# Kernel tuning notes

Measured on AMD Instinct MI355X. Metric: run time of the kernel, lower is better.

Reference implementation:

```python
import jax, jax.numpy as jnp
import numpy as np

NUM_HEADS = 8

def dwconv(x, w, b, pad):
    # depthwise conv: x [B, C, H, W], w [C, 1, k, k], groups=C
    y = jax.lax.conv_general_dilated(
        x, w, window_strides=(1, 1), padding=[(pad, pad), (pad, pad)],
        feature_group_count=x.shape[1], dimension_numbers=('NCHW', 'OIHW', 'NCHW'))
    return y + b[None, :, None, None]


def setup_inputs() -> dict:
    key = jax.random.key(0)
    ks = jax.random.split(key, 12)
    B, H, W = 32, 28, 28
    C = 512
    N = 1 + H * W
    Ch = C // NUM_HEADS  # 64
    s = lambda k, shp, fan: jax.random.normal(k, shp, jnp.float32) * (fan ** -0.5)
    return {
        'x': jax.random.normal(ks[0], (B, N, C), jnp.float32),
        'qkv_w': s(ks[1], (3 * C, C), C),
        'qkv_b': jnp.zeros((3 * C,), jnp.float32),
        'proj_w': s(ks[2], (C, C), C),
        'proj_b': jnp.zeros((C,), jnp.float32),
        'w3': s(ks[3], (2 * Ch, 1, 3, 3), 9),
        'b3': jnp.zeros((2 * Ch,), jnp.float32),
        'w5': s(ks[4], (3 * Ch, 1, 5, 5), 25),
        'b5': jnp.zeros((3 * Ch,), jnp.float32),
        'w7': s(ks[5], (3 * Ch, 1, 7, 7), 49),
        'b7': jnp.zeros((3 * Ch,), jnp.float32),
        'H': H,
        'W': W,
    }


def reference(x, qkv_w, qkv_b, proj_w, proj_b, w3, b3, w5, b5, w7, b7, H, W):
    B, N, C = x.shape
    h = NUM_HEADS
    Ch = C // h
    scale = Ch ** -0.5
    # qkv projection -> q, k, v each [B, h, N, Ch]
    qkv = (x @ qkv_w.T + qkv_b).reshape(B, N, 3, h, Ch).transpose(2, 0, 3, 1, 4)
    q, k, v = qkv[0], qkv[1], qkv[2]
    # factorized attention: softmax over tokens on k, then (k^T v) then q @ ...
    k_sm = jax.nn.softmax(k, axis=2)
    kv = jnp.einsum('bhnc,bhnd->bhcd', k_sm, v)          # [B,h,Ch,Ch]
    factor_att = jnp.einsum('bhnc,bhcd->bhnd', q, kv)    # [B,h,N,Ch]
    # conv relative position encoding (CRPE) on image tokens only
    q_img = q[:, :, 1:, :]                               # [B,h,HW,Ch]
    v_img = v[:, :, 1:, :].transpose(0, 1, 3, 2).reshape(B, h * Ch, H, W)
    splits = np.cumsum([2 * Ch, 3 * Ch, 3 * Ch])[:-1]
    v1, v2, v3 = jnp.split(v_img, splits, axis=1)
    conv_v = jnp.concatenate(
        [dwconv(v1, w3, b3, 1), dwconv(v2, w5, b5, 2), dwconv(v3, w7, b7, 3)], axis=1)
    conv_v = conv_v.reshape(B, h, Ch, H * W).transpose(0, 1, 3, 2)  # [B,h,HW,Ch]
    EV = q_img * conv_v
    crpe = jnp.pad(EV, ((0, 0), (0, 0), (1, 0), (0, 0)))  # zero row for cls token
    out = scale * factor_att + crpe
    out = out.transpose(0, 2, 1, 3).reshape(B, N, C)
    return out @ proj_w.T + proj_b
```

## Files before the change

kernel.cpp:

```cpp
#include <hip/hip_runtime.h>
#include <cstdint>
#include <cstddef>


typedef unsigned short u16;

#define HEADS 8
#define CHD   64
#define CDIM  512
#define NTOK  785
#define BATCH 32
#define MROWS (BATCH * NTOK)
#define MPAD  25344
#define QKVN  1536
#define IMGHW 784
#define KVSPLIT 7

typedef float  f32x4  __attribute__((ext_vector_type(4)));
typedef __bf16 bf16x8 __attribute__((ext_vector_type(8)));

__device__ __forceinline__ u16 f2bf(float f) {
  union { float f; uint32_t u; } x; x.f = f;
  uint32_t r = x.u + 0x7fffu + ((x.u >> 16) & 1u);
  return (u16)(r >> 16);
}
__device__ __forceinline__ float bf2f(u16 u) {
  union { uint32_t u; float f; } x; x.u = ((uint32_t)u) << 16;
  return x.f;
}
__device__ __forceinline__ uint32_t pk2(float a, float b) {
#if __has_builtin(__builtin_amdgcn_cvt_pk_bf16_f32)
  auto v = __builtin_amdgcn_cvt_pk_bf16_f32(a, b);
  union { decltype(v) v2; uint32_t u; } cv; cv.v2 = v; return cv.u;
#else
  return (uint32_t)f2bf(a) | ((uint32_t)f2bf(b) << 16);
#endif
}

__global__ __launch_bounds__(256)
void casts_kernel(const float* __restrict__ x, u16* __restrict__ xb,
                  const float* __restrict__ w1, u16* __restrict__ w1b,
                  const float* __restrict__ w2, u16* __restrict__ w2b) {
  const int N1 = MROWS * CDIM / 4, N2 = QKVN * CDIM / 4, N3 = CDIM * CDIM / 4;
  int i = blockIdx.x * 256 + threadIdx.x;
  const float* src; u16* dst;
  if (i < N1)           { src = x;  dst = xb;  }
  else if (i < N1 + N2) { i -= N1;  src = w1; dst = w1b; }
  else if (i < N1 + N2 + N3) { i -= N1 + N2; src = w2; dst = w2b; }
  else return;
  float4 v = reinterpret_cast<const float4*>(src)[i];
  uint2 o; o.x = pk2(v.x, v.y); o.y = pk2(v.z, v.w);
  reinterpret_cast<uint2*>(dst)[i] = o;
}

__device__ __forceinline__ void gld_lds16(const u16* g, u16* l) {
  __builtin_amdgcn_global_load_lds((__attribute__((address_space(1))) void*)g,
                                   (__attribute__((address_space(3))) void*)l,
                                   16, 0, 0);
}

template <int OUTBF16>
__global__ __launch_bounds__(512)
void gemm_bt(const u16* __restrict__ A, const u16* __restrict__ W,
             const float* __restrict__ bias, void* __restrict__ Cout,
             int Mstore, int N, int K, int nMt, int nNt) {
  __shared__ __align__(16) u16 lsA[2][256 * 32];
  __shared__ __align__(16) u16 lsB[2][128 * 32];
  const int flat = blockIdx.x;
  const int xcd = flat & 7, idx = flat >> 3;
  const int nt = idx % nNt;
  const int mt = (idx / nNt) * 8 + xcd;
  if (mt >= nMt) return;
  const int tile_m = mt * 256, tile_n = nt * 128;

  const int tid  = threadIdx.x;
  const int wave = tid >> 6, lane = tid & 63;
  const int quad = lane >> 4, l16 = lane & 15;
  const int wm = (wave & 3) * 64, wn = (wave >> 2) * 64;

  const int srow = tid >> 2;
  const int scol = ((tid & 3) ^ ((tid >> 3) & 3)) * 8;
  const int ldst = tid * 8;

  auto stage = [&](int kt, int buf) {
    const int kc = kt * 32 + scol;
#pragma unroll
    for (int s = 0; s < 2; ++s)
      gld_lds16(A + (size_t)(tile_m + s * 128 + srow) * K + kc,
                &lsA[buf][s * 4096 + ldst]);
    gld_lds16(W + (size_t)(tile_n + srow) * K + kc, &lsB[buf][ldst]);
  };

  f32x4 acc[4][4] = {};

  stage(0, 0);
  __syncthreads();

  const int KT = K >> 5;
  const int pch = (quad ^ ((l16 >> 1) & 3)) * 8;
#pragma unroll 2
  for (int t = 0; t < KT; ++t) {
    const int cur = t & 1;
    if (t + 1 < KT) stage(t + 1, cur ^ 1);
    bf16x8 af[4], bfr[4];
#pragma unroll
    for (int i = 0; i < 4; ++i) {
      af[i]  = *reinterpret_cast<const bf16x8*>(
          &lsA[cur][(wm + i * 16 + l16) * 32 + pch]);
      bfr[i] = *reinterpret_cast<const bf16x8*>(
          &lsB[cur][(wn + i * 16 + l16) * 32 + pch]);
    }
#pragma unroll
    for (int i = 0; i < 4; ++i)
#pragma unroll
      for (int j = 0; j < 4; ++j)
        acc[i][j] = __builtin_amdgcn_mfma_f32_16x16x32_bf16(
            af[i], bfr[j], acc[i][j], 0, 0, 0);
    __syncthreads();
  }

#pragma unroll
  for (int i = 0; i < 4; ++i) {
    const int mbase = tile_m + wm + i * 16 + quad * 4;
#pragma unroll
    for (int j = 0; j < 4; ++j) {
      const int n  = tile_n + wn + j * 16 + l16;
      const float bv = bias[n];
      const float v0 = acc[i][j][0] + bv, v1 = acc[i][j][1] + bv;
      const float v2 = acc[i][j][2] + bv, v3 = acc[i][j][3] + bv;
      if (OUTBF16) {
        u16* cp = reinterpret_cast<u16*>(Cout) + (size_t)mbase * N + n;
        const uint32_t p01 = pk2(v0, v1), p23 = pk2(v2, v3);
        if (mbase + 0 < Mstore) cp[0]            = (u16)p01;
        if (mbase + 1 < Mstore) cp[(size_t)N]    = (u16)(p01 >> 16);
        if (mbase + 2 < Mstore) cp[(size_t)N*2]  = (u16)p23;
        if (mbase + 3 < Mstore) cp[(size_t)N*3]  = (u16)(p23 >> 16);
      } else {
        float* cp = reinterpret_cast<float*>(Cout) + (size_t)mbase * N + n;
        if (mbase + 0 < Mstore) cp[0]           = v0;
        if (mbase + 1 < Mstore) cp[(size_t)N]   = v1;
        if (mbase + 2 < Mstore) cp[(size_t)N*2] = v2;
        if (mbase + 3 < Mstore) cp[(size_t)N*3] = v3;
      }
    }
  }
}

__global__ __launch_bounds__(256)
void kv_kernel(const u16* __restrict__ qkv, float* __restrict__ kvpart,
               float* __restrict__ kvsum) {
  const int bh = blockIdx.x, split = blockIdx.y;
  const int b = bh >> 3, h = bh & 7;
  const int n_start = split * 113;
  const int n_end = min(NTOK, n_start + 113);
  const int t = threadIdx.x;
  const int d = t & 63, cq = t >> 6;
  __shared__ float e_s[32 * 64];
  __shared__ float v_s[32 * 64];
  const u16* kbase = qkv + (size_t)(b * NTOK) * QKVN + CDIM + h * CHD;
  const u16* vbase = kbase + CDIM;
  float acc[16];
#pragma unroll
  for (int i = 0; i < 16; ++i) acc[i] = 0.f;
  float s_part = 0.f;

  for (int n0 = n_start; n0 < n_end; n0 += 32) {
    const int nc = min(32, n_end - n0);
    __syncthreads();
    for (int i = t; i < nc * 64; i += 256) {
      const int nl = i >> 6, c = i & 63;
      const float e = __expf(bf2f(kbase[(size_t)(n0 + nl) * QKVN + c]));
      e_s[i] = e; s_part += e;
      v_s[i] = bf2f(vbase[(size_t)(n0 + nl) * QKVN + c]);
    }
    __syncthreads();
    for (int nl = 0; nl < nc; ++nl) {
      const float vv = v_s[nl * 64 + d];
#pragma unroll
      for (int i = 0; i < 16; ++i)
        acc[i] += e_s[nl * 64 + cq * 16 + i] * vv;
    }
  }
#pragma unroll
  for (int i = 0; i < 16; ++i) {
    const int c = cq * 16 + i;
    kvpart[(((size_t)bh * KVSPLIT + split) * 64 + c) * 64 + d] = acc[i];
  }
  __syncthreads();
  e_s[t] = s_part;
  __syncthreads();
  if (t < 64)
    kvsum[((size_t)bh * KVSPLIT + split) * 64 + t] =
        e_s[t] + e_s[64 + t] + e_s[128 + t] + e_s[192 + t];
}

__global__ __launch_bounds__(256)
void kv_reduce_kernel(const float* __restrict__ kvpart, const float* __restrict__ kvsum,
                      u16* __restrict__ kvT) {
  const int bh = blockIdx.x;
  const int t = threadIdx.x;
  const int d = t & 63, cq = t >> 6;
#pragma unroll
  for (int cc = 0; cc < 16; ++cc) {
    const int c = cq * 16 + cc;
    float s = 0.f, S = 0.f;
#pragma unroll
    for (int sp = 0; sp < KVSPLIT; ++sp) {
      s += kvpart[(((size_t)bh * KVSPLIT + sp) * 64 + c) * 64 + d];
      S += kvsum[((size_t)bh * KVSPLIT + sp) * 64 + c];
    }
    kvT[(size_t)bh * 4096 + d * 64 + c] = f2bf(s / S);
  }
}

template <int KS>
__device__ __forceinline__ void conv_head(
    const u16* __restrict__ qkv, const float* __restrict__ wgt,
    const float* __restrict__ bias, int b, int head, int hh, int yt,
    u16* __restrict__ evbuf, u16* __restrict__ ls) {
  constexpr int PAD = KS / 2;
  constexpr int RIN = 4 + 2 * PAD;
  const int t = threadIdx.x;
  const int y0 = yt * 4;
  const u16* vimg = qkv + (size_t)(b * NTOK + 1) * QKVN + 2 * CDIM + head * 64;
  const int c8 = (t & 7) * 8;
  for (int pi = t >> 3; pi < RIN * 28; pi += 32) {
    const int ry = pi / 28, rx = pi - ry * 28;
    const int yy = y0 - PAD + ry;
    uint4 val = {0, 0, 0, 0};
    if (yy >= 0 && yy < 28)
      val = *reinterpret_cast<const uint4*>(vimg + (size_t)(yy * 28 + rx) * QKVN + c8);
    *reinterpret_cast<uint4*>(ls + pi * 64 + c8) = val;
  }
  __syncthreads();
  const int d = t & 63, yl = t >> 6;
  float wr[KS * KS];
  const float* wp = wgt + (hh * 64 + d) * KS * KS;
#pragma unroll
  for (int i = 0; i < KS * KS; ++i) wr[i] = wp[i];
  const float bv = bias[hh * 64 + d];
  float acc[28];
#pragma unroll
  for (int x = 0; x < 28; ++x) acc[x] = bv;
#pragma unroll
  for (int xx = 0; xx < 28; ++xx) {
    float col[KS];
#pragma unroll
    for (int r = 0; r < KS; ++r)
      col[r] = bf2f(ls[((yl + r) * 28 + xx) * 64 + d]);
#pragma unroll
    for (int j = 0; j < KS; ++j) {
      const int x = xx + PAD - j;
      if (x >= 0 && x < 28) {
#pragma unroll
        for (int r = 0; r < KS; ++r)
          acc[x] += col[r] * wr[r * KS + j];
      }
    }
  }
  const int p0 = (y0 + yl) * 28;
  const u16* qrow = qkv + (size_t)(b * NTOK + 1 + p0) * QKVN + head * 64 + d;
  u16* obase = evbuf + (((size_t)(b * 8 + head)) * IMGHW + p0) * 64 + d;
#pragma unroll
  for (int x = 0; x < 28; ++x) {
    const float ev = acc[x] * bf2f(qrow[(size_t)x * QKVN]);
    obase[(size_t)x * 64] = f2bf(ev);
  }
}

__global__ __launch_bounds__(256)
void conv_all_kernel(const u16* __restrict__ qkv,
                     const float* __restrict__ w3, const float* __restrict__ b3,
                     const float* __restrict__ w5, const float* __restrict__ b5,
                     const float* __restrict__ w7, const float* __restrict__ b7,
                     u16* __restrict__ evbuf) {
  __shared__ __align__(16) u16 ls[10 * 28 * 64];
  const int b = blockIdx.x, h = blockIdx.y, yt = blockIdx.z;
  if (h < 2)      conv_head<3>(qkv, w3, b3, b, h, h,     yt, evbuf, ls);
  else if (h < 5) conv_head<5>(qkv, w5, b5, b, h, h - 2, yt, evbuf, ls);
  else            conv_head<7>(qkv, w7, b7, b, h, h - 5, yt, evbuf, ls);
}

__global__ __launch_bounds__(256)
void combine_kernel(const u16* __restrict__ qkv, const u16* __restrict__ kvT,
                    const u16* __restrict__ evbuf, u16* __restrict__ attn) {
  const int bh = blockIdx.x;
  const int b = bh >> 3, h = bh & 7;
  const int wave = threadIdx.x >> 6, lane = threadIdx.x & 63;
  const int quad = lane >> 4, l16 = lane & 15;
  const int tokbase = blockIdx.y * 256 + wave * 64;

  const u16* kvb = kvT + (size_t)bh * 4096;
  bf16x8 bfr[4][2];
#pragma unroll
  for (int j = 0; j < 4; ++j)
#pragma unroll
    for (int kk = 0; kk < 2; ++kk)
      bfr[j][kk] = *reinterpret_cast<const bf16x8*>(
          &kvb[(j * 16 + l16) * 64 + kk * 32 + quad * 8]);

  bf16x8 af[4][2];
#pragma unroll
  for (int i = 0; i < 4; ++i) {
    const int tok = min(tokbase + i * 16 + l16, NTOK - 1);
    const u16* qrow = qkv + (size_t)(b * NTOK + tok) * QKVN + h * CHD;
    af[i][0] = *reinterpret_cast<const bf16x8*>(&qrow[quad * 8]);
    af[i][1] = *reinterpret_cast<const bf16x8*>(&qrow[32 + quad * 8]);
  }

  f32x4 acc[4][4] = {};
#pragma unroll
  for (int kk = 0; kk < 2; ++kk)
#pragma unroll
    for (int i = 0; i < 4; ++i)
#pragma unroll
      for (int j = 0; j < 4; ++j)
        acc[i][j] = __builtin_amdgcn_mfma_f32_16x16x32_bf16(af[i][kk], bfr[j][kk], acc[i][j], 0, 0, 0);

  const float scale = 0.125f;
  const u16* evb = evbuf + (size_t)bh * IMGHW * 64;
#pragma unroll
  for (int i = 0; i < 4; ++i) {
#pragma unroll
    for (int r = 0; r < 4; ++r) {
      const int tok = tokbase + i * 16 + quad * 4 + r;
      if (tok < NTOK) {
#pragma unroll
        for (int j = 0; j < 4; ++j) {
          const int d = j * 16 + l16;
          float out = scale * acc[i][j][r];
          if (tok > 0) out += bf2f(evb[(size_t)(tok - 1) * 64 + d]);
          attn[(size_t)(b * NTOK + tok) * CDIM + h * CHD + d] = f2bf(out);
        }
      }
    }
  }
}

extern "C" void kernel_launch(void* const* d_in, const int* in_sizes, int n_in,
                              void* d_out, int out_size, void* d_ws, size_t ws_size,
                              hipStream_t stream) {
  const float* x      = (const float*)d_in[0];
  const float* qkv_w  = (const float*)d_in[1];
  const float* qkv_b  = (const float*)d_in[2];
  const float* proj_w = (const float*)d_in[3];
  const float* proj_b = (const float*)d_in[4];
  const float* w3 = (const float*)d_in[5];
  const float* b3 = (const float*)d_in[6];
  const float* w5 = (const float*)d_in[7];
  const float* b5 = (const float*)d_in[8];
  const float* w7 = (const float*)d_in[9];
  const float* b7 = (const float*)d_in[10];
  float* out = (float*)d_out;

  char* p = (char*)d_ws;
  u16* xb    = (u16*)p;   p += (size_t)MPAD * CDIM * 2;
  u16* wqb   = (u16*)p;   p += (size_t)QKVN * CDIM * 2;
  u16* wpb   = (u16*)p;   p += (size_t)CDIM * CDIM * 2;
  u16* qkvb  = (u16*)p;   p += (size_t)MPAD * QKVN * 2;
  float* kvsum = (float*)p; p += (size_t)256 * KVSPLIT * 64 * 4;
  u16* kvT   = (u16*)p;   p += (size_t)256 * 64 * 64 * 2;
  char* shared_region = p;
  float* kvpart = (float*)shared_region;
  u16*   evbuf  = (u16*)shared_region;
  p += (size_t)256 * KVSPLIT * 64 * 64 * 4;
  u16* attn  = (u16*)p;   p += (size_t)MPAD * CDIM * 2;

  {
    const int total = MROWS * CDIM / 4 + QKVN * CDIM / 4 + CDIM * CDIM / 4;
    casts_kernel<<<(total + 255) / 256, 256, 0, stream>>>(x, xb, qkv_w, wqb, proj_w, wpb);
  }
  gemm_bt<1><<<13 * 8 * 12, 512, 0, stream>>>(xb, wqb, qkv_b, qkvb,
                                              MPAD, QKVN, CDIM, 99, 12);
  kv_kernel<<<dim3(256, KVSPLIT), 256, 0, stream>>>(qkvb, kvpart, kvsum);
  kv_reduce_kernel<<<256, 256, 0, stream>>>(kvpart, kvsum, kvT);
  conv_all_kernel<<<dim3(BATCH, HEADS, 7), 256, 0, stream>>>(
      qkvb, w3, b3, w5, b5, w7, b7, evbuf);
  combine_kernel<<<dim3(256, 4), 256, 0, stream>>>(qkvb, kvT, evbuf, attn);
  gemm_bt<0><<<13 * 8 * 4, 512, 0, stream>>>(attn, wpb, proj_b, out,
                                             MROWS, CDIM, CDIM, 99, 4);
}
```

Measured before the change: 327.3 us.

## Merge kv and conv kernels, vectorize loads, stage combine output via LDS

Folds the kv partial-sum kernel and the depthwise conv kernel into one launch, with grid rows split between the two jobs. The kv_reduce launch now follows both, so the two independent stages can overlap and their tail effects are shared. The kv loads become 4-wide, and conv weights are staged in shared memory so per-thread strided global weight reads are avoided. The combine kernel now goes through a swizzled LDS tile so it can write 16-byte coalesced bf16 rows instead of scattered 2-byte stores. evbuf now aliases the no-longer-needed xb buffer rather than kvpart, since both live at the same time. The costs are extra shared memory, which may reduce occupancy, and extra barriers in combine.

```diff
diff --git a/kernel.cpp b/kernel.cpp
--- a/kernel.cpp
+++ b/kernel.cpp
@@ -28,6 +28,8 @@
   union { uint32_t u; float f; } x; x.u = ((uint32_t)u) << 16;
   return x.f;
 }
+__device__ __forceinline__ float bflo(uint32_t u) { return bf2f((u16)(u & 0xffffu)); }
+__device__ __forceinline__ float bfhi(uint32_t u) { return bf2f((u16)(u >> 16)); }
 __device__ __forceinline__ uint32_t pk2(float a, float b) {
 #if __has_builtin(__builtin_amdgcn_cvt_pk_bf16_f32)
   auto v = __builtin_amdgcn_cvt_pk_bf16_f32(a, b);
@@ -146,39 +148,50 @@
   }
 }
 
-__global__ __launch_bounds__(256)
-void kv_kernel(const u16* __restrict__ qkv, float* __restrict__ kvpart,
-               float* __restrict__ kvsum) {
-  const int bh = blockIdx.x, split = blockIdx.y;
+__device__ __forceinline__ void kv_part(
+    const u16* __restrict__ qkv, float* __restrict__ kvpart,
+    float* __restrict__ kvsum, int bh, int split,
+    float* __restrict__ e_s, float* __restrict__ v_s) {
   const int b = bh >> 3, h = bh & 7;
   const int n_start = split * 113;
   const int n_end = min(NTOK, n_start + 113);
   const int t = threadIdx.x;
   const int d = t & 63, cq = t >> 6;
-  __shared__ float e_s[32 * 64];
-  __shared__ float v_s[32 * 64];
+  const int c4 = (t & 15) * 4;
   const u16* kbase = qkv + (size_t)(b * NTOK) * QKVN + CDIM + h * CHD;
   const u16* vbase = kbase + CDIM;
   float acc[16];
 #pragma unroll
   for (int i = 0; i < 16; ++i) acc[i] = 0.f;
-  float s_part = 0.f;
+  f32x4 sp4 = {0.f, 0.f, 0.f, 0.f};
 
   for (int n0 = n_start; n0 < n_end; n0 += 32) {
     const int nc = min(32, n_end - n0);
     __syncthreads();
-    for (int i = t; i < nc * 64; i += 256) {
-      const int nl = i >> 6, c = i & 63;
-      const float e = __expf(bf2f(kbase[(size_t)(n0 + nl) * QKVN + c]));
-      e_s[i] = e; s_part += e;
-      v_s[i] = bf2f(vbase[(size_t)(n0 + nl) * QKVN + c]);
+    for (int i4 = t; i4 < nc * 16; i4 += 256) {
+      const int nl = i4 >> 4;
+      const uint2 kk = *reinterpret_cast<const uint2*>(
+          &kbase[(size_t)(n0 + nl) * QKVN + c4]);
+      const uint2 vv = *reinterpret_cast<const uint2*>(
+          &vbase[(size_t)(n0 + nl) * QKVN + c4]);
+      f32x4 e4, v4;
+      e4[0] = __expf(bflo(kk.x)); e4[1] = __expf(bfhi(kk.x));
+      e4[2] = __expf(bflo(kk.y)); e4[3] = __expf(bfhi(kk.y));
+      v4[0] = bflo(vv.x); v4[1] = bfhi(vv.x);
+      v4[2] = bflo(vv.y); v4[3] = bfhi(vv.y);
+      *reinterpret_cast<f32x4*>(&e_s[nl * 64 + c4]) = e4;
+      *reinterpret_cast<f32x4*>(&v_s[nl * 64 + c4]) = v4;
+      sp4 += e4;
     }
     __syncthreads();
     for (int nl = 0; nl < nc; ++nl) {
       const float vv = v_s[nl * 64 + d];
-#pragma unroll
-      for (int i = 0; i < 16; ++i)
-        acc[i] += e_s[nl * 64 + cq * 16 + i] * vv;
+      const f32x4* ep = reinterpret_cast<const f32x4*>(&e_s[nl * 64 + cq * 16]);
+      const f32x4 e0 = ep[0], e1 = ep[1], e2 = ep[2], e3 = ep[3];
+      acc[0] += e0[0] * vv; acc[1] += e0[1] * vv; acc[2] += e0[2] * vv; acc[3] += e0[3] * vv;
+      acc[4] += e1[0] * vv; acc[5] += e1[1] * vv; acc[6] += e1[2] * vv; acc[7] += e1[3] * vv;
+      acc[8] += e2[0] * vv; acc[9] += e2[1] * vv; acc[10] += e2[2] * vv; acc[11] += e2[3] * vv;
+      acc[12] += e3[0] * vv; acc[13] += e3[1] * vv; acc[14] += e3[2] * vv; acc[15] += e3[3] * vv;
     }
   }
 #pragma unroll
@@ -187,11 +200,15 @@
     kvpart[(((size_t)bh * KVSPLIT + split) * 64 + c) * 64 + d] = acc[i];
   }
   __syncthreads();
-  e_s[t] = s_part;
+  *reinterpret_cast<f32x4*>(&e_s[t * 4]) = sp4;
   __syncthreads();
-  if (t < 64)
-    kvsum[((size_t)bh * KVSPLIT + split) * 64 + t] =
-        e_s[t] + e_s[64 + t] + e_s[128 + t] + e_s[192 + t];
+  if (t < 64) {
+    float S = 0.f;
+#pragma unroll
+    for (int m = 0; m < 16; ++m)
+      S += e_s[((t >> 2) + 16 * m) * 4 + (t & 3)];
+    kvsum[((size_t)bh * KVSPLIT + split) * 64 + t] = S;
+  }
 }
 
 __global__ __launch_bounds__(256)
@@ -217,12 +234,14 @@
 __device__ __forceinline__ void conv_head(
     const u16* __restrict__ qkv, const float* __restrict__ wgt,
     const float* __restrict__ bias, int b, int head, int hh, int yt,
-    u16* __restrict__ evbuf, u16* __restrict__ ls) {
+    u16* __restrict__ evbuf, u16* __restrict__ ls, float* __restrict__ wls) {
   constexpr int PAD = KS / 2;
   constexpr int RIN = 4 + 2 * PAD;
   const int t = threadIdx.x;
   const int y0 = yt * 4;
   const u16* vimg = qkv + (size_t)(b * NTOK + 1) * QKVN + 2 * CDIM + head * 64;
+  for (int i = t; i < 64 * KS * KS; i += 256)
+    wls[i] = wgt[hh * 64 * KS * KS + i];
   const int c8 = (t & 7) * 8;
   for (int pi = t >> 3; pi < RIN * 28; pi += 32) {
     const int ry = pi / 28, rx = pi - ry * 28;
@@ -235,9 +254,8 @@
   __syncthreads();
   const int d = t & 63, yl = t >> 6;
   float wr[KS * KS];
-  const float* wp = wgt + (hh * 64 + d) * KS * KS;
-#pragma unroll
-  for (int i = 0; i < KS * KS; ++i) wr[i] = wp[i];
+#pragma unroll
+  for (int i = 0; i < KS * KS; ++i) wr[i] = wls[d * KS * KS + i];
   const float bv = bias[hh * 64 + d];
   float acc[28];
 #pragma unroll
@@ -269,24 +287,36 @@
 }
 
 __global__ __launch_bounds__(256)
-void conv_all_kernel(const u16* __restrict__ qkv,
-                     const float* __restrict__ w3, const float* __restrict__ b3,
-                     const float* __restrict__ w5, const float* __restrict__ b5,
-                     const float* __restrict__ w7, const float* __restrict__ b7,
-                     u16* __restrict__ evbuf) {
-  __shared__ __align__(16) u16 ls[10 * 28 * 64];
-  const int b = blockIdx.x, h = blockIdx.y, yt = blockIdx.z;
-  if (h < 2)      conv_head<3>(qkv, w3, b3, b, h, h,     yt, evbuf, ls);
-  else if (h < 5) conv_head<5>(qkv, w5, b5, b, h, h - 2, yt, evbuf, ls);
-  else            conv_head<7>(qkv, w7, b7, b, h, h - 5, yt, evbuf, ls);
+void kv_conv_kernel(const u16* __restrict__ qkv, float* __restrict__ kvpart,
+                    float* __restrict__ kvsum,
+                    const float* __restrict__ w3, const float* __restrict__ b3,
+                    const float* __restrict__ w5, const float* __restrict__ b5,
+                    const float* __restrict__ w7, const float* __restrict__ b7,
+                    u16* __restrict__ evbuf) {
+  __shared__ __align__(16) char smem[10 * 28 * 64 * 2 + 64 * 49 * 4];
+  const int y = blockIdx.y;
+  if (y < KVSPLIT) {
+    float* e_s = reinterpret_cast<float*>(smem);
+    float* v_s = e_s + 32 * 64;
+    kv_part(qkv, kvpart, kvsum, blockIdx.x, y, e_s, v_s);
+  } else {
+    u16* ls = reinterpret_cast<u16*>(smem);
+    float* wls = reinterpret_cast<float*>(smem + 10 * 28 * 64 * 2);
+    const int b = blockIdx.x >> 3, h = blockIdx.x & 7, yt = y - KVSPLIT;
+    if (h < 2)      conv_head<3>(qkv, w3, b3, b, h, h,     yt, evbuf, ls, wls);
+    else if (h < 5) conv_head<5>(qkv, w5, b5, b, h, h - 2, yt, evbuf, ls, wls);
+    else            conv_head<7>(qkv, w7, b7, b, h, h - 5, yt, evbuf, ls, wls);
+  }
 }
 
 __global__ __launch_bounds__(256)
 void combine_kernel(const u16* __restrict__ qkv, const u16* __restrict__ kvT,
                     const u16* __restrict__ evbuf, u16* __restrict__ attn) {
+  __shared__ __align__(16) float sa[128 * 64];
   const int bh = blockIdx.x;
   const int b = bh >> 3, h = bh & 7;
-  const int wave = threadIdx.x >> 6, lane = threadIdx.x & 63;
+  const int t = threadIdx.x;
+  const int wave = t >> 6, lane = t & 63;
   const int quad = lane >> 4, l16 = lane & 15;
   const int tokbase = blockIdx.y * 256 + wave * 64;
 
@@ -320,20 +350,54 @@
   const float scale = 0.125f;
   const u16* evb = evbuf + (size_t)bh * IMGHW * 64;
 #pragma unroll
-  for (int i = 0; i < 4; ++i) {
-#pragma unroll
-    for (int r = 0; r < 4; ++r) {
-      const int tok = tokbase + i * 16 + quad * 4 + r;
+  for (int half = 0; half < 2; ++half) {
+    if ((wave >> 1) == half) {
+      const int rbase = (wave & 1) * 64;
+#pragma unroll
+      for (int i = 0; i < 4; ++i)
+#pragma unroll
+        for (int rr = 0; rr < 4; ++rr) {
+          const int rl = rbase + i * 16 + quad * 4 + rr;
+#pragma unroll
+          for (int j = 0; j < 4; ++j) {
+            const int dd = j * 16 + l16;
+            sa[rl * 64 + (((dd >> 2) ^ (rl & 15)) * 4) + (dd & 3)] =
+                scale * acc[i][j][rr];
+          }
+        }
+    }
+    __syncthreads();
+    {
+      const int rl = t >> 1;
+      const int tok = blockIdx.y * 256 + half * 128 + rl;
       if (tok < NTOK) {
-#pragma unroll
-        for (int j = 0; j < 4; ++j) {
-          const int d = j * 16 + l16;
-          float out = scale * acc[i][j][r];
-          if (tok > 0) out += bf2f(evb[(size_t)(tok - 1) * 64 + d]);
-          attn[(size_t)(b * NTOK + tok) * CDIM + h * CHD + d] = f2bf(out);
+        u16* orow = attn + (size_t)(b * NTOK + tok) * CDIM + h * CHD;
+        const int cb = (t & 1) * 8;
+#pragma unroll
+        for (int c2 = 0; c2 < 4; ++c2) {
+          const int ch0 = cb + c2 * 2;
+          const f32x4 v0 = *reinterpret_cast<const f32x4*>(
+              &sa[rl * 64 + ((ch0 ^ (rl & 15)) * 4)]);
+          const f32x4 v1 = *reinterpret_cast<const f32x4*>(
+              &sa[rl * 64 + (((ch0 + 1) ^ (rl & 15)) * 4)]);
+          float o0 = v0[0], o1 = v0[1], o2 = v0[2], o3 = v0[3];
+          float o4 = v1[0], o5 = v1[1], o6 = v1[2], o7 = v1[3];
+          if (tok > 0) {
+            const uint4 ev = *reinterpret_cast<const uint4*>(
+                &evb[(size_t)(tok - 1) * 64 + ch0 * 4]);
+            o0 += bflo(ev.x); o1 += bfhi(ev.x);
+            o2 += bflo(ev.y); o3 += bfhi(ev.y);
+            o4 += bflo(ev.z); o5 += bfhi(ev.z);
+            o6 += bflo(ev.w); o7 += bfhi(ev.w);
+          }
+          uint4 ow;
+          ow.x = pk2(o0, o1); ow.y = pk2(o2, o3);
+          ow.z = pk2(o4, o5); ow.w = pk2(o6, o7);
+          *reinterpret_cast<uint4*>(&orow[ch0 * 4]) = ow;
         }
       }
     }
+    __syncthreads();
   }
 }
 
@@ -360,11 +424,9 @@
   u16* qkvb  = (u16*)p;   p += (size_t)MPAD * QKVN * 2;
   float* kvsum = (float*)p; p += (size_t)256 * KVSPLIT * 64 * 4;
   u16* kvT   = (u16*)p;   p += (size_t)256 * 64 * 64 * 2;
-  char* shared_region = p;
-  float* kvpart = (float*)shared_region;
-  u16*   evbuf  = (u16*)shared_region;
-  p += (size_t)256 * KVSPLIT * 64 * 64 * 4;
+  float* kvpart = (float*)p; p += (size_t)256 * KVSPLIT * 64 * 64 * 4;
   u16* attn  = (u16*)p;   p += (size_t)MPAD * CDIM * 2;
+  u16* evbuf = xb;
 
   {
     const int total = MROWS * CDIM / 4 + QKVN * CDIM / 4 + CDIM * CDIM / 4;
@@ -372,10 +434,9 @@
   }
   gemm_bt<1><<<13 * 8 * 12, 512, 0, stream>>>(xb, wqb, qkv_b, qkvb,
                                               MPAD, QKVN, CDIM, 99, 12);
-  kv_kernel<<<dim3(256, KVSPLIT), 256, 0, stream>>>(qkvb, kvpart, kvsum);
+  kv_conv_kernel<<<dim3(256, KVSPLIT + 7), 256, 0, stream>>>(
+      qkvb, kvpart, kvsum, w3, b3, w5, b5, w7, b7, evbuf);
   kv_reduce_kernel<<<256, 256, 0, stream>>>(kvpart, kvsum, kvT);
-  conv_all_kernel<<<dim3(BATCH, HEADS, 7), 256, 0, stream>>>(
-      qkvb, w3, b3, w5, b5, w7, b7, evbuf);
   combine_kernel<<<dim3(256, 4), 256, 0, stream>>>(qkvb, kvT, evbuf, attn);
   gemm_bt<0><<<13 * 8 * 4, 512, 0, stream>>>(attn, wpb, proj_b, out,
                                              MROWS, CDIM, CDIM, 99, 4);
```

New measurement: 313.1 us. 1.05x faster.
